# Kernel optimization log

Hardware: AMD Instinct MI355X
Metric: run time of the kernel (lower is better)

## Reference

```python
import jax, jax.numpy as jnp
import numpy as np

B, N, ND, D, K = 2, 5000, 3, 128, 6

def _lin_init(key, fan_in, fan_out):
    # torch nn.Linear default: U(-1/sqrt(fan_in), 1/sqrt(fan_in)) for W and b
    k1, k2 = jax.random.split(key)
    bound = 1.0 / np.sqrt(fan_in)
    W = jax.random.uniform(k1, (fan_in, fan_out), minval=-bound, maxval=bound, dtype=jnp.float32)
    b = jax.random.uniform(k2, (fan_out,), minval=-bound, maxval=bound, dtype=jnp.float32)
    return W, b

def setup_inputs() -> dict:
    key = jax.random.key(0)
    ks = jax.random.split(key, 7)
    loc = jax.random.uniform(ks[0], (B, N, 2), dtype=jnp.float32)
    deadline = jax.random.uniform(ks[1], (B, N), dtype=jnp.float32)
    depot = jax.random.uniform(ks[2], (B, 2), dtype=jnp.float32)
    W_init, b_init = _lin_init(ks[3], ND, D)      # init_embed: 3 -> 128
    W_nbr, b_nbr = _lin_init(ks[4], ND, D)        # neighbour_encode: 3 -> 128
    W_depot, b_depot = _lin_init(ks[5], 2, D)     # init_embed_depot: 2 -> 128
    W_final, b_final = _lin_init(ks[6], D, D)     # final_embedding: 128 -> 128
    return {"loc": loc, "deadline": deadline, "depot": depot,
            "W_init": W_init, "b_init": b_init,
            "W_nbr": W_nbr, "b_nbr": b_nbr,
            "W_depot": W_depot, "b_depot": b_depot,
            "W_final": W_final, "b_final": b_final}

def reference(loc, deadline, depot, W_init, b_init, W_nbr, b_nbr, W_depot, b_depot, W_final, b_final):
    x = jnp.concatenate([loc, deadline[:, :, None]], axis=2)          # [B,N,3]
    x2 = x[:, :, 0:2]                                                 # [B,N,2]
    F0 = x @ W_init + b_init                                          # [B,N,D]
    # pairwise L2 distances [B,N,N]
    dist = jnp.linalg.norm(x2[:, None, :, :] - x2[:, :, None, :], axis=-1)
    neighbors = jnp.argsort(dist, axis=-1)[:, :, :K]                  # [B,N,K]
    # faithful to torch `x[:, neighbors][0]`: gather features from batch 0
    neighbour = x[0][neighbors]                                       # [B,N,K,3]
    neighbour_delta = neighbour - x[:, :, None, :]                    # [B,N,K,3]
    nd_emb = neighbour_delta @ W_nbr + b_nbr                          # [B,N,K,D]
    concat = jnp.concatenate([F0[:, :, None, :], nd_emb], axis=2)     # [B,N,K+1,D]
    F_final = (concat @ W_final + b_final).sum(axis=2)                # [B,N,D]
    depot_emb = (depot @ W_depot + b_depot)[:, None, :]               # [B,1,D]
    h = jnp.concatenate([depot_emb, F_final], axis=1)                 # [B,N+1,D]
    return h, h.mean(axis=1)
```

## Files before the change

kernel.cpp:

```cpp
#include <hip/hip_runtime.h>
#include <hip/hip_bf16.h>

#define NB 2
#define NPTS 5000
#define DIM 128
#define G 64
#define NCELL (G*G)
#define HCELL (1.0f/G)
#define MEAN_OFF (2*5001*128)

#define WS_INT_F 41024
#define OFF_CSTART 0
#define OFF_CURSOR (NB*(NCELL+1))
#define OFF_PTSJ   (OFF_CURSOR + NB*NCELL)
#define N_INTS     (OFF_PTSJ + NB*NPTS)
#define WS_XY_F    (WS_INT_F + N_INTS)

__global__ __launch_bounds__(256) void pre_kernel(
    const float* __restrict__ W_init, const float* __restrict__ b_init,
    const float* __restrict__ W_nbr,  const float* __restrict__ b_nbr,
    const float* __restrict__ W_depot,const float* __restrict__ b_depot,
    const float* __restrict__ W_final,const float* __restrict__ b_final,
    const float* __restrict__ depot,
    float* __restrict__ ws, float* __restrict__ out) {
  const int tid = threadIdx.x;
  int* __restrict__ cz = (int*)(ws + WS_INT_F) + OFF_CURSOR;
  for (int idx = tid; idx < NB*NCELL; idx += 256) cz[idx] = 0;
  for (int idx = tid; idx < 768; idx += 256) {
    const float* Ws = (idx < 384) ? W_init : W_nbr;
    int rem = (idx >= 384) ? idx - 384 : idx;
    int t = rem >> 7, d = rem & 127;
    float acc = 0.f;
#pragma unroll 8
    for (int e = 0; e < 128; ++e) acc += Ws[t*128 + e] * W_final[e*128 + d];
    ws[idx] = acc;
  }
  if (tid < 128) {
    float acc = 0.f;
#pragma unroll 8
    for (int e = 0; e < 128; ++e) acc += (b_init[e] + 6.f*b_nbr[e]) * W_final[e*128 + tid];
    ws[768 + tid] = acc + 7.f*b_final[tid];
  }
  {
    int b = tid >> 7, d = tid & 127;
    float val = depot[b*2] * W_depot[d] + depot[b*2+1] * W_depot[128 + d] + b_depot[d];
    out[(size_t)b*5001*128 + d] = val;
    out[MEAN_OFF + b*128 + d]   = val * (1.f/5001.f);
  }
}

__device__ __forceinline__ int cell_of(float v) {
  int c = (int)(v * (float)G);
  return c < 0 ? 0 : (c > G-1 ? G-1 : c);
}

__global__ __launch_bounds__(256) void count_kernel(
    const float* __restrict__ loc, int* __restrict__ ints) {
  int tid = blockIdx.x*256 + threadIdx.x;
  if (tid >= NB*NPTS) return;
  int b = tid >= NPTS;
  float2 p = ((const float2*)loc)[tid];
  int c = cell_of(p.y)*G + cell_of(p.x);
  atomicAdd(&ints[OFF_CURSOR + b*NCELL + c], 1);
}

__global__ __launch_bounds__(1024) void scan_kernel(int* __restrict__ ints) {
  const int b = blockIdx.x, t = threadIdx.x;
  __shared__ int part[1024];
  int* cnt = ints + OFF_CURSOR + b*NCELL;
  int* cst = ints + OFF_CSTART + b*(NCELL+1);
  int c0 = cnt[4*t], c1 = cnt[4*t+1], c2 = cnt[4*t+2], c3 = cnt[4*t+3];
  int tot = c0+c1+c2+c3;
  part[t] = tot;
  __syncthreads();
  for (int off = 1; off < 1024; off <<= 1) {
    int v = (t >= off) ? part[t-off] : 0;
    __syncthreads();
    part[t] += v;
    __syncthreads();
  }
  int base = part[t] - tot;
  cst[4*t]   = base;            cnt[4*t]   = base;
  cst[4*t+1] = base+c0;         cnt[4*t+1] = base+c0;
  cst[4*t+2] = base+c0+c1;      cnt[4*t+2] = base+c0+c1;
  cst[4*t+3] = base+c0+c1+c2;   cnt[4*t+3] = base+c0+c1+c2;
  if (t == 1023) cst[NCELL] = part[1023];
}

__global__ __launch_bounds__(256) void scatter_kernel(
    const float* __restrict__ loc, int* __restrict__ ints,
    float2* __restrict__ xy) {
  int tid = blockIdx.x*256 + threadIdx.x;
  if (tid >= NB*NPTS) return;
  int b = tid >= NPTS;
  int i = tid - b*NPTS;
  float2 p = ((const float2*)loc)[tid];
  int c = cell_of(p.y)*G + cell_of(p.x);
  int pos = atomicAdd(&ints[OFF_CURSOR + b*NCELL + c], 1);
  xy[b*NPTS + pos] = p;
  ints[OFF_PTSJ + b*NPTS + pos] = i;
}

#define PACK(d_, j_) ((((unsigned long long)__float_as_uint(d_)) << 32) | (unsigned)(j_))
#define KINIT 0x7f800000ffffffffULL
#define INS6(nk) \
  { bool c_; unsigned long long t_; \
    c_ = nk<k0; t_=k0; k0=c_?nk:k0; nk=c_?t_:nk; \
    c_ = nk<k1; t_=k1; k1=c_?nk:k1; nk=c_?t_:nk; \
    c_ = nk<k2; t_=k2; k2=c_?nk:k2; nk=c_?t_:nk; \
    c_ = nk<k3; t_=k3; k3=c_?nk:k3; nk=c_?t_:nk; \
    c_ = nk<k4; t_=k4; k4=c_?nk:k4; nk=c_?t_:nk; \
    c_ = nk<k5; k5=c_?nk:k5; }

__global__ __launch_bounds__(256) void knn_grid(
    const float* __restrict__ loc, const float* __restrict__ deadline,
    const int* __restrict__ ints, const float2* __restrict__ xy,
    float* __restrict__ nbrsum) {
  const int b = blockIdx.y;
  __shared__ float2 sxy[NPTS];
  __shared__ int    sj[NPTS];
  const float2* XY = xy + b*NPTS;
  const int*    J  = ints + OFF_PTSJ + b*NPTS;
  for (int k = threadIdx.x; k < NPTS; k += 256) { sxy[k] = XY[k]; sj[k] = J[k]; }
  __syncthreads();

  const int s = blockIdx.x*256 + threadIdx.x;
  if (s >= NPTS) return;
  const int* cs = ints + OFF_CSTART + b*(NCELL+1);

  const float2 q = sxy[s];
  const int qi = sj[s];
  const int cx = cell_of(q.x), cy = cell_of(q.y);

  unsigned long long k0=KINIT,k1=KINIT,k2=KINIT,k3=KINIT,k4=KINIT,k5=KINIT;

#define SCAN_CELL(cidx) \
  { int p0 = cs[cidx], p1 = cs[(cidx)+1]; \
    for (int p = p0; p < p1; ++p) { \
      float2 t = sxy[p]; \
      float dx = q.x - t.x, dy = q.y - t.y; \
      float ss = __fadd_rn(__fmul_rn(dx,dx), __fmul_rn(dy,dy)); \
      float nd = sqrtf(ss); \
      unsigned long long nk = PACK(nd, (unsigned)sj[p]); \
      if (nk < k5) { INS6(nk); } } }

  {
    int x0 = cx-2 < 0 ? 0 : cx-2, x1 = cx+2 > G-1 ? G-1 : cx+2;
    int y0 = cy-2 < 0 ? 0 : cy-2, y1 = cy+2 > G-1 ? G-1 : cy+2;
    for (int y = y0; y <= y1; ++y)
      for (int x = x0; x <= x1; ++x) SCAN_CELL(y*G + x);
  }
  int Rb = 2;
  while (true) {
    float d6 = __uint_as_float((unsigned)(k5 >> 32));
    if (0.999999f * ((float)Rb * HCELL) > d6) break;
    ++Rb;
    if (Rb > G) break;
    int xa = cx-Rb < 0 ? 0 : cx-Rb, xb = cx+Rb > G-1 ? G-1 : cx+Rb;
    int yt = cy-Rb, yb = cy+Rb;
    if (yt >= 0)   { for (int x = xa; x <= xb; ++x) SCAN_CELL(yt*G + x); }
    if (yb <= G-1) { for (int x = xa; x <= xb; ++x) SCAN_CELL(yb*G + x); }
    int ya = cy-Rb+1 < 0 ? 0 : cy-Rb+1, yz = cy+Rb-1 > G-1 ? G-1 : cy+Rb-1;
    if (cx-Rb >= 0)   { for (int y = ya; y <= yz; ++y) SCAN_CELL(y*G + (cx-Rb)); }
    if (cx+Rb <= G-1) { for (int y = ya; y <= yz; ++y) SCAN_CELL(y*G + (cx+Rb)); }
  }

  float s0=0.f, s1=0.f, s2=0.f;
  { int j=(int)(unsigned)k0; s0+=loc[j*2]; s1+=loc[j*2+1]; s2+=deadline[j]; }
  { int j=(int)(unsigned)k1; s0+=loc[j*2]; s1+=loc[j*2+1]; s2+=deadline[j]; }
  { int j=(int)(unsigned)k2; s0+=loc[j*2]; s1+=loc[j*2+1]; s2+=deadline[j]; }
  { int j=(int)(unsigned)k3; s0+=loc[j*2]; s1+=loc[j*2+1]; s2+=deadline[j]; }
  { int j=(int)(unsigned)k4; s0+=loc[j*2]; s1+=loc[j*2+1]; s2+=deadline[j]; }
  { int j=(int)(unsigned)k5; s0+=loc[j*2]; s1+=loc[j*2+1]; s2+=deadline[j]; }
  const size_t o = ((size_t)b*NPTS + qi) * 4;
  nbrsum[o] = s0; nbrsum[o+1] = s1; nbrsum[o+2] = s2;
}

__global__ __launch_bounds__(256) void rows_kernel(
    const float* __restrict__ loc, const float* __restrict__ deadline,
    const float* __restrict__ ws, float* __restrict__ out) {
  const int b  = blockIdx.y;
  const int d  = threadIdx.x & 127;
  const int rs = threadIdx.x >> 7;
  const float A0 = ws[d],      A1 = ws[128+d], A2 = ws[256+d];
  const float B0 = ws[384+d],  B1 = ws[512+d], B2 = ws[640+d];
  const float cc = ws[768+d];
  const float* __restrict__ nbrsum = ws + 1024;
  float msum = 0.f;
#pragma unroll
  for (int it = 0; it < 8; ++it) {
    int i = blockIdx.x*16 + it*2 + rs;
    if (i < NPTS) {
      size_t r = (size_t)b*NPTS + i;
      float u0 = loc[r*2], u1 = loc[r*2+1], u2 = deadline[r];
      float w0 = nbrsum[r*4]   - 6.f*u0;
      float w1 = nbrsum[r*4+1] - 6.f*u1;
      float w2 = nbrsum[r*4+2] - 6.f*u2;
      float val = cc + u0*A0 + u1*A1 + u2*A2 + w0*B0 + w1*B1 + w2*B2;
      out[((size_t)b*5001 + 1 + i)*128 + d] = val;
      msum += val;
    }
  }
  atomicAdd(&out[MEAN_OFF + b*128 + d], msum * (1.f/5001.f));
}

extern "C" void kernel_launch(void* const* d_in, const int* in_sizes, int n_in,
                              void* d_out, int out_size, void* d_ws, size_t ws_size,
                              hipStream_t stream) {
  const float* loc      = (const float*)d_in[0];
  const float* deadline = (const float*)d_in[1];
  const float* depot    = (const float*)d_in[2];
  const float* W_init   = (const float*)d_in[3];
  const float* b_init   = (const float*)d_in[4];
  const float* W_nbr    = (const float*)d_in[5];
  const float* b_nbr    = (const float*)d_in[6];
  const float* W_depot  = (const float*)d_in[7];
  const float* b_depot  = (const float*)d_in[8];
  const float* W_final  = (const float*)d_in[9];
  const float* b_final  = (const float*)d_in[10];
  float* out = (float*)d_out;
  float* ws  = (float*)d_ws;
  int*    ints = (int*)(ws + WS_INT_F);
  float2* xy   = (float2*)(ws + WS_XY_F);

  hipLaunchKernelGGL(pre_kernel, dim3(1), dim3(256), 0, stream,
                     W_init, b_init, W_nbr, b_nbr, W_depot, b_depot,
                     W_final, b_final, depot, ws, out);
  hipLaunchKernelGGL(count_kernel, dim3((NB*NPTS + 255)/256), dim3(256), 0, stream,
                     loc, ints);
  hipLaunchKernelGGL(scan_kernel, dim3(NB), dim3(1024), 0, stream, ints);
  hipLaunchKernelGGL(scatter_kernel, dim3((NB*NPTS + 255)/256), dim3(256), 0, stream,
                     loc, ints, xy);
  hipLaunchKernelGGL(knn_grid, dim3((NPTS + 255)/256, NB), dim3(256), 0, stream,
                     loc, deadline, ints, xy, ws + 1024);
  hipLaunchKernelGGL(rows_kernel, dim3((NPTS + 15)/16, NB), dim3(256), 0, stream,
                     loc, deadline, ws, out);
}
```

Baseline: 159.5 us.

## Split weight-fold across blocks and scan grid rows as contiguous ranges

```diff
diff --git a/kernel.cpp b/kernel.cpp
--- a/kernel.cpp
+++ b/kernel.cpp
@@ -24,22 +24,35 @@
     const float* __restrict__ depot,
     float* __restrict__ ws, float* __restrict__ out) {
   const int tid = threadIdx.x;
-  int* __restrict__ cz = (int*)(ws + WS_INT_F) + OFF_CURSOR;
-  for (int idx = tid; idx < NB*NCELL; idx += 256) cz[idx] = 0;
-  for (int idx = tid; idx < 768; idx += 256) {
+  const int blk = blockIdx.x;
+  if (blk < 3) {
+    int idx = blk*256 + tid;
     const float* Ws = (idx < 384) ? W_init : W_nbr;
     int rem = (idx >= 384) ? idx - 384 : idx;
     int t = rem >> 7, d = rem & 127;
-    float acc = 0.f;
+    float a0=0.f, a1=0.f, a2=0.f, a3=0.f;
 #pragma unroll 8
-    for (int e = 0; e < 128; ++e) acc += Ws[t*128 + e] * W_final[e*128 + d];
-    ws[idx] = acc;
-  }
+    for (int e = 0; e < 128; e += 4) {
+      a0 += Ws[t*128 + e]   * W_final[(e)*128 + d];
+      a1 += Ws[t*128 + e+1] * W_final[(e+1)*128 + d];
+      a2 += Ws[t*128 + e+2] * W_final[(e+2)*128 + d];
+      a3 += Ws[t*128 + e+3] * W_final[(e+3)*128 + d];
+    }
+    ws[idx] = (a0+a1)+(a2+a3);
+    return;
+  }
+  int* __restrict__ cz = (int*)(ws + WS_INT_F) + OFF_CURSOR;
+  for (int idx = tid; idx < NB*NCELL; idx += 256) cz[idx] = 0;
   if (tid < 128) {
-    float acc = 0.f;
+    float a0=0.f, a1=0.f, a2=0.f, a3=0.f;
 #pragma unroll 8
-    for (int e = 0; e < 128; ++e) acc += (b_init[e] + 6.f*b_nbr[e]) * W_final[e*128 + tid];
-    ws[768 + tid] = acc + 7.f*b_final[tid];
+    for (int e = 0; e < 128; e += 4) {
+      a0 += (b_init[e]   + 6.f*b_nbr[e])   * W_final[(e)*128 + tid];
+      a1 += (b_init[e+1] + 6.f*b_nbr[e+1]) * W_final[(e+1)*128 + tid];
+      a2 += (b_init[e+2] + 6.f*b_nbr[e+2]) * W_final[(e+2)*128 + tid];
+      a3 += (b_init[e+3] + 6.f*b_nbr[e+3]) * W_final[(e+3)*128 + tid];
+    }
+    ws[768 + tid] = (a0+a1)+(a2+a3) + 7.f*b_final[tid];
   }
   {
     int b = tid >> 7, d = tid & 127;
@@ -112,6 +125,15 @@
     c_ = nk<k4; t_=k4; k4=c_?nk:k4; nk=c_?t_:nk; \
     c_ = nk<k5; k5=c_?nk:k5; }
 
+#define SCAN_RANGE(p0_, p1_) \
+  for (int p = (p0_); p < (p1_); ++p) { \
+    float2 t = sxy[p]; \
+    float dx = q.x - t.x, dy = q.y - t.y; \
+    float ss = __fadd_rn(__fmul_rn(dx,dx), __fmul_rn(dy,dy)); \
+    float nd = sqrtf(ss); \
+    unsigned long long nk = PACK(nd, (unsigned)sj[p]); \
+    if (nk < k5) { INS6(nk); } }
+
 __global__ __launch_bounds__(256) void knn_grid(
     const float* __restrict__ loc, const float* __restrict__ deadline,
     const int* __restrict__ ints, const float2* __restrict__ xy,
@@ -126,30 +148,30 @@
 
   const int s = blockIdx.x*256 + threadIdx.x;
   if (s >= NPTS) return;
-  const int* cs = ints + OFF_CSTART + b*(NCELL+1);
+  const int* __restrict__ cs = ints + OFF_CSTART + b*(NCELL+1);
 
   const float2 q = sxy[s];
   const int qi = sj[s];
   const int cx = cell_of(q.x), cy = cell_of(q.y);
+  const int x0 = cx-2 < 0 ? 0 : cx-2, x1 = cx+2 > G-1 ? G-1 : cx+2;
 
   unsigned long long k0=KINIT,k1=KINIT,k2=KINIT,k3=KINIT,k4=KINIT,k5=KINIT;
 
-#define SCAN_CELL(cidx) \
-  { int p0 = cs[cidx], p1 = cs[(cidx)+1]; \
-    for (int p = p0; p < p1; ++p) { \
-      float2 t = sxy[p]; \
-      float dx = q.x - t.x, dy = q.y - t.y; \
-      float ss = __fadd_rn(__fmul_rn(dx,dx), __fmul_rn(dy,dy)); \
-      float nd = sqrtf(ss); \
-      unsigned long long nk = PACK(nd, (unsigned)sj[p]); \
-      if (nk < k5) { INS6(nk); } } }
-
+  int rb0,re0,rb1,re1,rb2,re2,rb3,re3,rb4,re4;
   {
-    int x0 = cx-2 < 0 ? 0 : cx-2, x1 = cx+2 > G-1 ? G-1 : cx+2;
-    int y0 = cy-2 < 0 ? 0 : cy-2, y1 = cy+2 > G-1 ? G-1 : cy+2;
-    for (int y = y0; y <= y1; ++y)
-      for (int x = x0; x <= x1; ++x) SCAN_CELL(y*G + x);
-  }
+    int y;
+    y = cy-2; if (y >= 0 && y <= G-1) { rb0 = cs[y*G+x0]; re0 = cs[y*G+x1+1]; } else { rb0 = 0; re0 = 0; }
+    y = cy-1; if (y >= 0 && y <= G-1) { rb1 = cs[y*G+x0]; re1 = cs[y*G+x1+1]; } else { rb1 = 0; re1 = 0; }
+    y = cy;                           { rb2 = cs[y*G+x0]; re2 = cs[y*G+x1+1]; }
+    y = cy+1; if (y >= 0 && y <= G-1) { rb3 = cs[y*G+x0]; re3 = cs[y*G+x1+1]; } else { rb3 = 0; re3 = 0; }
+    y = cy+2; if (y >= 0 && y <= G-1) { rb4 = cs[y*G+x0]; re4 = cs[y*G+x1+1]; } else { rb4 = 0; re4 = 0; }
+  }
+  SCAN_RANGE(rb0, re0);
+  SCAN_RANGE(rb1, re1);
+  SCAN_RANGE(rb2, re2);
+  SCAN_RANGE(rb3, re3);
+  SCAN_RANGE(rb4, re4);
+
   int Rb = 2;
   while (true) {
     float d6 = __uint_as_float((unsigned)(k5 >> 32));
@@ -158,11 +180,11 @@
     if (Rb > G) break;
     int xa = cx-Rb < 0 ? 0 : cx-Rb, xb = cx+Rb > G-1 ? G-1 : cx+Rb;
     int yt = cy-Rb, yb = cy+Rb;
-    if (yt >= 0)   { for (int x = xa; x <= xb; ++x) SCAN_CELL(yt*G + x); }
-    if (yb <= G-1) { for (int x = xa; x <= xb; ++x) SCAN_CELL(yb*G + x); }
+    if (yt >= 0)   { int p0 = cs[yt*G+xa], p1 = cs[yt*G+xb+1]; SCAN_RANGE(p0, p1); }
+    if (yb <= G-1) { int p0 = cs[yb*G+xa], p1 = cs[yb*G+xb+1]; SCAN_RANGE(p0, p1); }
     int ya = cy-Rb+1 < 0 ? 0 : cy-Rb+1, yz = cy+Rb-1 > G-1 ? G-1 : cy+Rb-1;
-    if (cx-Rb >= 0)   { for (int y = ya; y <= yz; ++y) SCAN_CELL(y*G + (cx-Rb)); }
-    if (cx+Rb <= G-1) { for (int y = ya; y <= yz; ++y) SCAN_CELL(y*G + (cx+Rb)); }
+    if (cx-Rb >= 0)   { for (int y = ya; y <= yz; ++y) { int p0 = cs[y*G+(cx-Rb)], p1 = cs[y*G+(cx-Rb)+1]; SCAN_RANGE(p0, p1); } }
+    if (cx+Rb <= G-1) { for (int y = ya; y <= yz; ++y) { int p0 = cs[y*G+(cx+Rb)], p1 = cs[y*G+(cx+Rb)+1]; SCAN_RANGE(p0, p1); } }
   }
 
   float s0=0.f, s1=0.f, s2=0.f;
@@ -223,7 +245,7 @@
   int*    ints = (int*)(ws + WS_INT_F);
   float2* xy   = (float2*)(ws + WS_XY_F);
 
-  hipLaunchKernelGGL(pre_kernel, dim3(1), dim3(256), 0, stream,
+  hipLaunchKernelGGL(pre_kernel, dim3(4), dim3(256), 0, stream,
                      W_init, b_init, W_nbr, b_nbr, W_depot, b_depot,
                      W_final, b_final, depot, ws, out);
   hipLaunchKernelGGL(count_kernel, dim3((NB*NPTS + 255)/256), dim3(256), 0, stream,
```

Result: faster. 133.9 us (-16.0%).
